# Performance work log

Measured on AMD Instinct MI355X. Metric: run time of the kernel, lower is better.

## Reference

```python
import jax, jax.numpy as jnp
import numpy as np

B, H, Q, K = 2, 12, 2048, 2048
D, NPOS = 128, 512


def setup_inputs() -> dict:
    key = jax.random.key(0)
    k1, k2, k3 = jax.random.split(key, 3)
    return {
        "query": jax.random.normal(k1, (B, H, Q, D), dtype=jnp.float32),
        "attn_logits": jax.random.normal(k2, (B, H, Q, K), dtype=jnp.float32),
        "pos_emb": jax.random.normal(k3, (1, D, NPOS), dtype=jnp.float32),
        "npos_max": NPOS,
    }


def reference(query, attn_logits, pos_emb, npos_max):
    # CoPE, 1D (H=None) branch.
    gates = jax.nn.sigmoid(attn_logits)                       # [b,h,q,k]
    # reversed cumsum along keys: position of each key counted from the right
    pos = jnp.flip(jnp.cumsum(jnp.flip(gates, axis=-1), axis=-1), axis=-1)
    pos = jnp.minimum(pos, jnp.float32(npos_max - 1))
    pos_ceil = jnp.ceil(pos).astype(jnp.int32)                # [b,h,q,k]
    pos_floor = jnp.floor(pos).astype(jnp.int32)
    # query @ pos_emb -> interpolation table over integer positions
    logits_int = jnp.einsum("bhqd,dn->bhqn", query, pos_emb[0])  # [b,h,q,npos]
    logits_ceil = jnp.take_along_axis(logits_int, pos_ceil, axis=-1)
    logits_floor = jnp.take_along_axis(logits_int, pos_floor, axis=-1)
    w = pos - pos_floor.astype(pos.dtype)
    return logits_ceil * w + logits_floor * (1.0 - w)
```

## Files before the change

kernel.cpp:

```cpp
#include <hip/hip_runtime.h>
#include <math.h>

#define DD    128
#define NPOS  512
#define KK    2048
#define RPB   16
#define BLK   1024

typedef __attribute__((ext_vector_type(8))) short short8_t;
typedef __attribute__((ext_vector_type(4))) float f32x4;

union BfPack {
    unsigned u[4];
    short8_t v;
};

__device__ __forceinline__ float sigmoidf_fast(float x) {
    return 1.0f / (1.0f + __expf(-x));
}

__device__ __forceinline__ unsigned pack_bf16(float lo, float hi) {
    return (__float_as_uint(hi) & 0xffff0000u) | (__float_as_uint(lo) >> 16);
}

__global__ __launch_bounds__(BLK, 8)
void cope_kernel(const float* __restrict__ query,
                 const float* __restrict__ attn,
                 const float* __restrict__ pos_emb,
                 const int*   __restrict__ npos_max_p,
                 float* __restrict__ out)
{
    const int t    = threadIdx.x;
    const int wv   = t >> 6;
    const int lane = t & 63;

    __shared__ float s_tab[RPB][NPOS + 1];

    const size_t row_base = (size_t)blockIdx.x * RPB;

    {
        const int m  = lane & 15;
        const int g  = lane >> 4;
        const int n0 = wv * 32 + m;

        f32x4 acc0 = {0.f, 0.f, 0.f, 0.f};
        f32x4 acc1 = {0.f, 0.f, 0.f, 0.f};

        #pragma unroll
        for (int kk = 0; kk < 4; ++kk) {
            const int k0 = kk * 32 + g * 8;

            const float* qp = query + (row_base + m) * DD + k0;
            f32x4 a0 = *reinterpret_cast<const f32x4*>(qp);
            f32x4 a1 = *reinterpret_cast<const f32x4*>(qp + 4);
            BfPack af;
            af.u[0] = pack_bf16(a0.x, a0.y);
            af.u[1] = pack_bf16(a0.z, a0.w);
            af.u[2] = pack_bf16(a1.x, a1.y);
            af.u[3] = pack_bf16(a1.z, a1.w);

            const float* bp = pos_emb + (size_t)k0 * NPOS + n0;
            float b0[8], b1[8];
            #pragma unroll
            for (int j = 0; j < 8; ++j) {
                b0[j] = bp[(size_t)j * NPOS];
                b1[j] = bp[(size_t)j * NPOS + 16];
            }
            BfPack bf0, bf1;
            #pragma unroll
            for (int j = 0; j < 4; ++j) {
                bf0.u[j] = pack_bf16(b0[2 * j], b0[2 * j + 1]);
                bf1.u[j] = pack_bf16(b1[2 * j], b1[2 * j + 1]);
            }

            acc0 = __builtin_amdgcn_mfma_f32_16x16x32_bf16(af.v, bf0.v, acc0, 0, 0, 0);
            acc1 = __builtin_amdgcn_mfma_f32_16x16x32_bf16(af.v, bf1.v, acc1, 0, 0, 0);
        }

        #pragma unroll
        for (int r = 0; r < 4; ++r) {
            s_tab[g * 4 + r][n0]      = acc0[r];
            s_tab[g * 4 + r][n0 + 16] = acc1[r];
        }
        if (t < RPB) s_tab[t][NPOS] = 0.0f;
    }
    __syncthreads();

    const size_t row = row_base + wv;
    const float* arow = attn + row * (size_t)KK;
    float*       orow = out  + row * (size_t)KK;
    const float* tab  = s_tab[wv];

    const float clampv = (float)(*npos_max_p - 1);

    float suff[8][4];
    float lct[8];
    float incl[8];

    #pragma unroll
    for (int c = 0; c < 8; ++c) {
        f32x4 gv = *reinterpret_cast<const f32x4*>(arow + c * 256 + lane * 4);
        float s0 = sigmoidf_fast(gv.x);
        float s1 = sigmoidf_fast(gv.y);
        float s2 = sigmoidf_fast(gv.z);
        float s3 = sigmoidf_fast(gv.w);
        suff[c][3] = s3;
        suff[c][2] = s2 + suff[c][3];
        suff[c][1] = s1 + suff[c][2];
        suff[c][0] = s0 + suff[c][1];
        lct[c] = suff[c][0];

        float v = lct[c];
        #pragma unroll
        for (int off = 1; off < 64; off <<= 1) {
            float u = __shfl_down(v, off);
            if (lane + off < 64) v += u;
        }
        incl[c] = v;
    }

    float Tc[8];
    #pragma unroll
    for (int c = 0; c < 8; ++c) Tc[c] = __shfl(incl[c], 0);
    float offc[8];
    offc[7] = 0.0f;
    #pragma unroll
    for (int c = 6; c >= 0; --c) offc[c] = offc[c + 1] + Tc[c + 1];

    #pragma unroll
    for (int c = 0; c < 8; ++c) {
        float base = offc[c] + (incl[c] - lct[c]);
        f32x4 res;
        #pragma unroll
        for (int j = 0; j < 4; ++j) {
            float pos = fminf(suff[c][j] + base, clampv);
            int   ifl = (int)pos;
            float wgt = pos - (float)ifl;
            float lf  = tab[ifl];
            float lc  = tab[ifl + 1];
            res[j] = fmaf(wgt, lc - lf, lf);
        }
        __builtin_nontemporal_store(res, reinterpret_cast<f32x4*>(orow + c * 256 + lane * 4));
    }
}

extern "C" void kernel_launch(void* const* d_in, const int* in_sizes, int n_in,
                              void* d_out, int out_size, void* d_ws, size_t ws_size,
                              hipStream_t stream) {
    const float* query   = (const float*)d_in[0];
    const float* attn    = (const float*)d_in[1];
    const float* pos_emb = (const float*)d_in[2];
    const int*   nposp   = (const int*)d_in[3];
    float*       outp    = (float*)d_out;

    const int rows   = in_sizes[1] / KK;
    const int blocks = rows / RPB;

    cope_kernel<<<blocks, BLK, 0, stream>>>(query, attn, pos_emb, nposp, outp);
}
```

Baseline: 185.9 us.

## Halve block size so each wave handles two rows and four MFMA column tiles

The block shrinks from 1024 to 512 threads. Each of the 8 waves now computes four 16-column MFMA tiles of the position table instead of two, and then runs the sigmoid/suffix-scan/interpolation pass over two attention rows in sequence. The attention loads become nontemporal, and the clamped positions are folded into the suffix registers ahead of the gather loop. The aim is to cut per-block overhead and change occupancy and scheduling, at the cost of more serial work per wave and higher register pressure.

Result: slower. 200.9 us (+8.1%).

```diff
diff --git a/kernel.cpp b/kernel.cpp
--- a/kernel.cpp
+++ b/kernel.cpp
@@ -5,7 +5,7 @@
 #define NPOS  512
 #define KK    2048
 #define RPB   16
-#define BLK   1024
+#define BLK   512
 
 typedef __attribute__((ext_vector_type(8))) short short8_t;
 typedef __attribute__((ext_vector_type(4))) float f32x4;
@@ -41,10 +41,11 @@
     {
         const int m  = lane & 15;
         const int g  = lane >> 4;
-        const int n0 = wv * 32 + m;
+        const int nb = wv * 64 + m;
 
-        f32x4 acc0 = {0.f, 0.f, 0.f, 0.f};
-        f32x4 acc1 = {0.f, 0.f, 0.f, 0.f};
+        f32x4 acc[4];
+        #pragma unroll
+        for (int nt = 0; nt < 4; ++nt) acc[nt] = (f32x4){0.f, 0.f, 0.f, 0.f};
 
         #pragma unroll
         for (int kk = 0; kk < 4; ++kk) {
@@ -59,88 +60,96 @@
             af.u[2] = pack_bf16(a1.x, a1.y);
             af.u[3] = pack_bf16(a1.z, a1.w);
 
-            const float* bp = pos_emb + (size_t)k0 * NPOS + n0;
-            float b0[8], b1[8];
             #pragma unroll
-            for (int j = 0; j < 8; ++j) {
-                b0[j] = bp[(size_t)j * NPOS];
-                b1[j] = bp[(size_t)j * NPOS + 16];
+            for (int nt = 0; nt < 4; ++nt) {
+                const float* bp = pos_emb + (size_t)k0 * NPOS + nb + nt * 16;
+                float b[8];
+                #pragma unroll
+                for (int j = 0; j < 8; ++j)
+                    b[j] = bp[(size_t)j * NPOS];
+                BfPack bf;
+                #pragma unroll
+                for (int j = 0; j < 4; ++j)
+                    bf.u[j] = pack_bf16(b[2 * j], b[2 * j + 1]);
+                acc[nt] = __builtin_amdgcn_mfma_f32_16x16x32_bf16(af.v, bf.v, acc[nt], 0, 0, 0);
             }
-            BfPack bf0, bf1;
-            #pragma unroll
-            for (int j = 0; j < 4; ++j) {
-                bf0.u[j] = pack_bf16(b0[2 * j], b0[2 * j + 1]);
-                bf1.u[j] = pack_bf16(b1[2 * j], b1[2 * j + 1]);
-            }
-
-            acc0 = __builtin_amdgcn_mfma_f32_16x16x32_bf16(af.v, bf0.v, acc0, 0, 0, 0);
-            acc1 = __builtin_amdgcn_mfma_f32_16x16x32_bf16(af.v, bf1.v, acc1, 0, 0, 0);
         }
 
         #pragma unroll
-        for (int r = 0; r < 4; ++r) {
-            s_tab[g * 4 + r][n0]      = acc0[r];
-            s_tab[g * 4 + r][n0 + 16] = acc1[r];
-        }
+        for (int nt = 0; nt < 4; ++nt)
+            #pragma unroll
+            for (int r = 0; r < 4; ++r)
+                s_tab[g * 4 + r][nb + nt * 16] = acc[nt][r];
+
         if (t < RPB) s_tab[t][NPOS] = 0.0f;
     }
     __syncthreads();
 
-    const size_t row = row_base + wv;
-    const float* arow = attn + row * (size_t)KK;
-    float*       orow = out  + row * (size_t)KK;
-    const float* tab  = s_tab[wv];
-
     const float clampv = (float)(*npos_max_p - 1);
 
-    float suff[8][4];
-    float lct[8];
-    float incl[8];
+    #pragma unroll
+    for (int rr = 0; rr < 2; ++rr) {
+        const int    trow = wv + rr * 8;
+        const size_t row  = row_base + trow;
+        const float* arow = attn + row * (size_t)KK;
+        float*       orow = out  + row * (size_t)KK;
+        const float* tab  = s_tab[trow];
 
-    #pragma unroll
-    for (int c = 0; c < 8; ++c) {
-        f32x4 gv = *reinterpret_cast<const f32x4*>(arow + c * 256 + lane * 4);
-        float s0 = sigmoidf_fast(gv.x);
-        float s1 = sigmoidf_fast(gv.y);
-        float s2 = sigmoidf_fast(gv.z);
-        float s3 = sigmoidf_fast(gv.w);
-        suff[c][3] = s3;
-        suff[c][2] = s2 + suff[c][3];
-        suff[c][1] = s1 + suff[c][2];
-        suff[c][0] = s0 + suff[c][1];
-        lct[c] = suff[c][0];
+        f32x4 suff[8];
+        float lct[8];
+        float incl[8];
 
-        float v = lct[c];
         #pragma unroll
-        for (int off = 1; off < 64; off <<= 1) {
-            float u = __shfl_down(v, off);
-            if (lane + off < 64) v += u;
+        for (int c = 0; c < 8; ++c) {
+            f32x4 gv = __builtin_nontemporal_load(
+                reinterpret_cast<const f32x4*>(arow + c * 256 + lane * 4));
+            float s0 = sigmoidf_fast(gv.x);
+            float s1 = sigmoidf_fast(gv.y);
+            float s2 = sigmoidf_fast(gv.z);
+            float s3 = sigmoidf_fast(gv.w);
+            suff[c][3] = s3;
+            suff[c][2] = s2 + s3;
+            suff[c][1] = s1 + suff[c][2];
+            suff[c][0] = s0 + suff[c][1];
+            lct[c] = suff[c][0];
+
+            float v = lct[c];
+            #pragma unroll
+            for (int off = 1; off < 64; off <<= 1) {
+                float u = __shfl_down(v, off);
+                if (lane + off < 64) v += u;
+            }
+            incl[c] = v;
         }
-        incl[c] = v;
-    }
 
-    float Tc[8];
-    #pragma unroll
-    for (int c = 0; c < 8; ++c) Tc[c] = __shfl(incl[c], 0);
-    float offc[8];
-    offc[7] = 0.0f;
-    #pragma unroll
-    for (int c = 6; c >= 0; --c) offc[c] = offc[c + 1] + Tc[c + 1];
+        float Tc[8];
+        #pragma unroll
+        for (int c = 0; c < 8; ++c) Tc[c] = __shfl(incl[c], 0);
+        float offc = 0.0f;
+        #pragma unroll
+        for (int c = 7; c >= 0; --c) {
+            float base = offc + (incl[c] - lct[c]);
+            #pragma unroll
+            for (int j = 0; j < 4; ++j)
+                suff[c][j] = fminf(suff[c][j] + base, clampv);
+            offc += Tc[c];
+        }
 
-    #pragma unroll
-    for (int c = 0; c < 8; ++c) {
-        float base = offc[c] + (incl[c] - lct[c]);
-        f32x4 res;
         #pragma unroll
-        for (int j = 0; j < 4; ++j) {
-            float pos = fminf(suff[c][j] + base, clampv);
-            int   ifl = (int)pos;
-            float wgt = pos - (float)ifl;
-            float lf  = tab[ifl];
-            float lc  = tab[ifl + 1];
-            res[j] = fmaf(wgt, lc - lf, lf);
+        for (int c = 0; c < 8; ++c) {
+            f32x4 res;
+            #pragma unroll
+            for (int j = 0; j < 4; ++j) {
+                float pos = suff[c][j];
+                int   ifl = (int)pos;
+                float wgt = pos - (float)ifl;
+                float lf  = tab[ifl];
+                float lc  = tab[ifl + 1];
+                res[j] = fmaf(wgt, lc - lf, lf);
+            }
+            __builtin_nontemporal_store(res,
+                reinterpret_cast<f32x4*>(orow + c * 256 + lane * 4));
         }
-        __builtin_nontemporal_store(res, reinterpret_cast<f32x4*>(orow + c * 256 + lane * 4));
     }
 }
 
```
